# Optimization experiments

Measured on AMD Instinct MI355X. Metric: run time of the kernel, lower is better.

The kernel has to match this reference:

```python
import jax, jax.numpy as jnp
import numpy as np

D_MODEL = 768
H = 12
D_K = D_MODEL // H
D_FF = 3072
B, S = 1, 4096


def setup_inputs() -> dict:
    key = jax.random.key(0)
    ks = jax.random.split(key, 16)
    sd = 0.02
    inp = {
        'x': jax.random.normal(ks[0], (B, S, D_MODEL), jnp.float32),
        'mask': jnp.ones((B, 1, S, S), jnp.int32),
        'wq': jax.random.normal(ks[1], (D_MODEL, D_MODEL), jnp.float32) * sd,
        'bq': jnp.zeros((D_MODEL,), jnp.float32),
        'wk': jax.random.normal(ks[2], (D_MODEL, D_MODEL), jnp.float32) * sd,
        'bk': jnp.zeros((D_MODEL,), jnp.float32),
        'wv': jax.random.normal(ks[3], (D_MODEL, D_MODEL), jnp.float32) * sd,
        'bv': jnp.zeros((D_MODEL,), jnp.float32),
        'wo': jax.random.normal(ks[4], (D_MODEL, D_MODEL), jnp.float32) * sd,
        'bo': jnp.zeros((D_MODEL,), jnp.float32),
        'w1': jax.random.normal(ks[5], (D_MODEL, D_FF), jnp.float32) * sd,
        'b1': jnp.zeros((D_FF,), jnp.float32),
        'w2': jax.random.normal(ks[6], (D_FF, D_MODEL), jnp.float32) * sd,
        'b2': jnp.zeros((D_MODEL,), jnp.float32),
    }
    return inp


def _mha(x, mask, wq, bq, wk, bk, wv, bv, wo, bo):
    b, s, _ = x.shape
    q = (x @ wq + bq).reshape(b, s, H, D_K).transpose(0, 2, 1, 3)  # (b,h,s,dk)
    k = (x @ wk + bk).reshape(b, s, H, D_K).transpose(0, 2, 1, 3)
    v = (x @ wv + bv).reshape(b, s, H, D_K).transpose(0, 2, 1, 3)
    scores = jnp.einsum('bhqd,bhkd->bhqk', q, k) / jnp.sqrt(jnp.float32(D_K))
    scores = jnp.where(mask == 0, jnp.float32(-1e9), scores)
    p = jax.nn.softmax(scores, axis=-1)  # dropout disabled (eval)
    ctx = jnp.einsum('bhqk,bhkd->bhqd', p, v)
    ctx = ctx.transpose(0, 2, 1, 3).reshape(b, s, D_MODEL)
    return ctx @ wo + bo


def reference(x, mask, wq, bq, wk, bk, wv, bv, wo, bo, w1, b1, w2, b2):
    # residual 1: self-attention (SkipConnection applies no LayerNorm in forward)
    x = x + _mha(x, mask, wq, bq, wk, bk, wv, bv, wo, bo)
    # residual 2: feed-forward (relu), dropout disabled
    ff = jax.nn.relu(x @ w1 + b1) @ w2 + b2
    return x + ff
```

## Files before the change

kernel.cpp:

```cpp
#include <hip/hip_runtime.h>


typedef __attribute__((ext_vector_type(4))) float f32x4;
typedef __attribute__((ext_vector_type(8))) short bf16x8;

#define MFMA(a, b, c) __builtin_amdgcn_mfma_f32_16x16x32_bf16((a), (b), (c), 0, 0, 0)

__device__ inline ushort f2b(float f) {
  union { float f; unsigned u; } v; v.f = f;
  unsigned r = v.u + 0x7fffu + ((v.u >> 16) & 1u);
  return (ushort)(r >> 16);
}

__device__ inline unsigned cvt_pk_bf16(float lo, float hi) {
  unsigned r;
  asm("v_cvt_pk_bf16_f32 %0, %1, %2" : "=v"(r) : "v"(lo), "v"(hi));
  return r;
}

__device__ inline float fexp2(float x) {
  float r;
  asm("v_exp_f32 %0, %1" : "=v"(r) : "v"(x));
  return r;
}

__device__ inline void gl_lds16(const ushort* g, ushort* l) {
  __builtin_amdgcn_global_load_lds(
      (const __attribute__((address_space(1))) unsigned int*)g,
      (__attribute__((address_space(3))) unsigned int*)l, 16, 0, 0);
}


__global__ void cvt_f2b_kernel(const float* __restrict__ in, ushort* __restrict__ out, int n) {
  int i = (blockIdx.x * blockDim.x + threadIdx.x) * 4;
  if (i < n) {
    float4 v = *(const float4*)&in[i];
    ushort4 o; o.x = f2b(v.x); o.y = f2b(v.y); o.z = f2b(v.z); o.w = f2b(v.w);
    *(ushort4*)&out[i] = o;
  }
}

__global__ void tr_f2b_kernel(const float* __restrict__ in, ushort* __restrict__ out, int K, int N) {
  __shared__ float tile[32][33];
  const int kb = blockIdx.x * 32, nb = blockIdx.y * 32;
  const int tx = threadIdx.x, ty = threadIdx.y;
#pragma unroll
  for (int i = 0; i < 32; i += 8)
    tile[ty + i][tx] = in[(size_t)(kb + ty + i) * N + nb + tx];
  __syncthreads();
#pragma unroll
  for (int i = 0; i < 32; i += 8)
    out[(size_t)(nb + ty + i) * K + kb + tx] = f2b(tile[tx][ty + i]);
}

__global__ void concat3_kernel(const float* __restrict__ a, const float* __restrict__ b,
                               const float* __restrict__ c, float* __restrict__ o) {
  int i = blockIdx.x * 256 + threadIdx.x;
  if (i < 2304) o[i] = (i < 768) ? a[i] : (i < 1536) ? b[i - 768] : c[i - 1536];
}

template <int EPI, int BM, int BN>
__global__ __launch_bounds__(256, 2) void gemm_bt(
    const ushort* __restrict__ A, const ushort* __restrict__ Bt,
    const float* __restrict__ bias, const float* __restrict__ res,
    float* __restrict__ outF, ushort* __restrict__ outB, ushort* __restrict__ outV,
    int M, int N, int K) {
  constexpr int IM = BM / 32;
  constexpr int JN = BN / 32;
  __shared__ __align__(16) ushort As[2][BM * 32];
  __shared__ __align__(16) ushort Bs[2][BN * 32];
  const int t = threadIdx.x;
  const int wave = t >> 6, lane = t & 63;
  const int lr = lane & 15, lg = lane >> 4;
  const int wm = (wave >> 1) * (BM / 2), wn = (wave & 1) * (BN / 2);
  const int bm = blockIdx.x * BM, bn = blockIdx.y * BN;

  f32x4 acc[IM][JN] = {};

  const ushort* Ab = A + (size_t)bm * K;
  const ushort* Bb = Bt + (size_t)bn * K;
  const int srow = t >> 2;
  const int scol = (t & 3) * 8;

  auto STAGE = [&](int buf, int k0) {
#pragma unroll
    for (int rr = 0; rr < BM; rr += 64)
      gl_lds16(Ab + (size_t)(srow + rr) * K + k0 + scol, &As[buf][rr * 32 + t * 8]);
#pragma unroll
    for (int rr = 0; rr < BN; rr += 64)
      gl_lds16(Bb + (size_t)(srow + rr) * K + k0 + scol, &Bs[buf][rr * 32 + t * 8]);
  };

  STAGE(0, 0);
  __syncthreads();
  int cur = 0;

  for (int k0 = 0; k0 < K; k0 += 32) {
    if (k0 + 32 < K) STAGE(cur ^ 1, k0 + 32);

    bf16x8 af[IM], bfr[JN];
#pragma unroll
    for (int i = 0; i < IM; ++i)
      af[i] = *(const bf16x8*)&As[cur][(wm + i * 16 + lr) * 32 + lg * 8];
#pragma unroll
    for (int j = 0; j < JN; ++j)
      bfr[j] = *(const bf16x8*)&Bs[cur][(wn + j * 16 + lr) * 32 + lg * 8];
#pragma unroll
    for (int i = 0; i < IM; ++i)
#pragma unroll
      for (int j = 0; j < JN; ++j)
        acc[i][j] = MFMA(af[i], bfr[j], acc[i][j]);

    __syncthreads();
    cur ^= 1;
  }

#pragma unroll
  for (int j = 0; j < JN; ++j) {
    const int col = bn + wn + j * 16 + lr;
    const float bv = bias[col];
#pragma unroll
    for (int i = 0; i < IM; ++i) {
      const int row0 = bm + wm + i * 16 + lg * 4;
      float v[4];
#pragma unroll
      for (int r = 0; r < 4; ++r) {
        v[r] = acc[i][j][r] + bv;
        if (EPI == 2) v[r] = fmaxf(v[r], 0.f);
        if (EPI == 1 || EPI == 3) v[r] += res[(size_t)(row0 + r) * N + col];
        if (EPI == 1 || EPI == 3) outF[(size_t)(row0 + r) * N + col] = v[r];
      }
      if (EPI == 0) {
        if (col < 1536) {
#pragma unroll
          for (int r = 0; r < 4; ++r) outB[(size_t)(row0 + r) * 1536 + col] = f2b(v[r]);
        } else {
          ushort4 pk;
          pk.x = f2b(v[0]); pk.y = f2b(v[1]); pk.z = f2b(v[2]); pk.w = f2b(v[3]);
          *(ushort4*)&outV[(size_t)(col - 1536) * 4096 + row0] = pk;
        }
      } else if (EPI == 1 || EPI == 2) {
#pragma unroll
        for (int r = 0; r < 4; ++r) outB[(size_t)(row0 + r) * N + col] = f2b(v[r]);
      }
    }
  }
}

__global__ __launch_bounds__(512, 6) void attn_kernel(
    const ushort* __restrict__ qk, const ushort* __restrict__ vg,
    ushort* __restrict__ Opart, float2* __restrict__ stats) {
  __shared__ __align__(16) ushort Ks[2][64 * 64];
  __shared__ __align__(16) ushort Vt[64 * 64];
  __shared__ __align__(16) ushort Ps[8][16 * 72];
  const int h = blockIdx.y;
  const int qb = blockIdx.x * 128;
  const int kb0 = blockIdx.z * 2048;
  const int t = threadIdx.x, wave = t >> 6, lane = t & 63;
  const int lr = lane & 15, lg = lane >> 4;
  constexpr float SC = 0.18033688011112042f;

  const ushort* Qp = qk + (size_t)(qb + wave * 16 + lr) * 1536 + 64 * h;
  const bf16x8 qf0 = *(const bf16x8*)(Qp + lg * 8);
  const bf16x8 qf1 = *(const bf16x8*)(Qp + 32 + lg * 8);

  f32x4 oacc[4] = {};
  float m = -1e30f, lsum = 0.f;

  const int srow = t >> 3;
  const int schunk = ((t & 7) ^ (srow & 7)) * 8;
  const ushort* Kp0 = qk + (size_t)srow * 1536 + 768 + 64 * h + schunk;
  const ushort* Vp0 = vg + (size_t)(64 * h + srow) * 4096 + schunk;
  const int swr = lr & 7;

  auto STAGE_K = [&](int buf, int kb) {
    gl_lds16(Kp0 + (size_t)kb * 1536, &Ks[buf][t * 8]);
  };
  auto STAGE_V = [&](int kb) {
    gl_lds16(Vp0 + kb, &Vt[t * 8]);
  };

  STAGE_K(0, kb0);
  __syncthreads();
  int cur = 0;

  for (int kb = kb0; kb < kb0 + 2048; kb += 64) {
    if (kb + 64 < kb0 + 2048) STAGE_K(cur ^ 1, kb + 64);
    STAGE_V(kb);

    const ushort* Kc = Ks[cur];

    float p[16];
    __builtin_amdgcn_s_setprio(1);
#pragma unroll
    for (int kt = 0; kt < 4; ++kt) {
      const int kr = kt * 16 + lr;
      bf16x8 ka0 = *(const bf16x8*)&Kc[kr * 64 + ((lg ^ swr) * 8)];
      bf16x8 ka1 = *(const bf16x8*)&Kc[kr * 64 + (((lg + 4) ^ swr) * 8)];
      f32x4 s = {};
      s = MFMA(ka0, qf0, s);
      s = MFMA(ka1, qf1, s);
#pragma unroll
      for (int r = 0; r < 4; ++r) p[kt * 4 + r] = s[r];
    }
    __builtin_amdgcn_s_setprio(0);

    float mx = fmaxf(fmaxf(p[0], p[1]), p[2]);
    mx = fmaxf(fmaxf(mx, p[3]), p[4]);
    mx = fmaxf(fmaxf(mx, p[5]), p[6]);
    mx = fmaxf(fmaxf(mx, p[7]), p[8]);
    mx = fmaxf(fmaxf(mx, p[9]), p[10]);
    mx = fmaxf(fmaxf(mx, p[11]), p[12]);
    mx = fmaxf(fmaxf(mx, p[13]), p[14]);
    mx = fmaxf(mx, p[15]);
    mx = fmaxf(mx, __shfl_xor(mx, 16));
    mx = fmaxf(mx, __shfl_xor(mx, 32));
    mx *= SC;

    if (!__all(mx <= m + 8.0f)) {
      const float alpha = fexp2(m - mx);
      lsum *= alpha;
      float al[4];
#pragma unroll
      for (int r = 0; r < 4; ++r) al[r] = __shfl(alpha, lg * 4 + r);
#pragma unroll
      for (int dt = 0; dt < 4; ++dt)
#pragma unroll
        for (int r = 0; r < 4; ++r) oacc[dt][r] *= al[r];
      m = mx;
    }

#pragma unroll
    for (int i = 0; i < 16; ++i) p[i] = fexp2(fmaf(p[i], SC, -m));

    ushort* Pw = Ps[wave];
#pragma unroll
    for (int kt = 0; kt < 4; ++kt) {
      uint2 pk;
      pk.x = cvt_pk_bf16(p[kt * 4 + 0], p[kt * 4 + 1]);
      pk.y = cvt_pk_bf16(p[kt * 4 + 2], p[kt * 4 + 3]);
      *(uint2*)&Pw[lr * 72 + kt * 16 + lg * 4] = pk;
    }

    float ts = ((p[0] + p[1]) + (p[2] + p[3])) + ((p[4] + p[5]) + (p[6] + p[7]));
    ts += ((p[8] + p[9]) + (p[10] + p[11])) + ((p[12] + p[13]) + (p[14] + p[15]));
    ts += __shfl_xor(ts, 16);
    ts += __shfl_xor(ts, 32);
    lsum += ts;

    __syncthreads();

    bf16x8 pa0 = *(const bf16x8*)&Pw[lr * 72 + lg * 8];
    bf16x8 pa1 = *(const bf16x8*)&Pw[lr * 72 + 32 + lg * 8];
    __builtin_amdgcn_s_setprio(1);
#pragma unroll
    for (int dt = 0; dt < 4; ++dt) {
      const int vd = dt * 16 + lr;
      bf16x8 vb0 = *(const bf16x8*)&Vt[vd * 64 + ((lg ^ swr) * 8)];
      bf16x8 vb1 = *(const bf16x8*)&Vt[vd * 64 + (((lg + 4) ^ swr) * 8)];
      oacc[dt] = MFMA(pa0, vb0, oacc[dt]);
      oacc[dt] = MFMA(pa1, vb1, oacc[dt]);
    }
    __builtin_amdgcn_s_setprio(0);

    __syncthreads();
    cur ^= 1;
  }

  float li[4];
#pragma unroll
  for (int r = 0; r < 4; ++r) li[r] = __shfl(lsum, lg * 4 + r);
  ushort* Os = Opart + (size_t)blockIdx.z * 3145728;
#pragma unroll
  for (int dt = 0; dt < 4; ++dt)
#pragma unroll
    for (int r = 0; r < 4; ++r) {
      const int row = qb + wave * 16 + lg * 4 + r;
      const int col = 64 * h + dt * 16 + lr;
      Os[(size_t)row * 768 + col] = f2b(oacc[dt][r] / li[r]);
    }
  if (lane < 16) {
    float2 st; st.x = m; st.y = lsum;
    stats[(size_t)blockIdx.z * 49152 + (size_t)(qb + wave * 16 + lane) * 12 + h] = st;
  }
}

__global__ void attn_combine_kernel(const ushort* __restrict__ Op,
                                    const float2* __restrict__ st,
                                    ushort* __restrict__ ctx) {
  const int i = blockIdx.x * 256 + threadIdx.x;
  const int q = i / 96, cc = i - q * 96;
  const int h = cc >> 3;
  const float2 s0 = st[(size_t)q * 12 + h];
  const float2 s1 = st[49152 + (size_t)q * 12 + h];
  const float M = fmaxf(s0.x, s1.x);
  const float w0 = fexp2(s0.x - M) * s0.y;
  const float w1 = fexp2(s1.x - M) * s1.y;
  const float ri = 1.0f / (w0 + w1);
  const float a0 = w0 * ri, a1 = w1 * ri;
  const size_t off = (size_t)q * 768 + cc * 8;
  const uint4 ua = *(const uint4*)(Op + off);
  const uint4 ub = *(const uint4*)(Op + 3145728 + off);
  const uint* pa = (const uint*)&ua;
  const uint* pb = (const uint*)&ub;
  uint out[4];
#pragma unroll
  for (int j = 0; j < 4; ++j) {
    const float fa0 = __uint_as_float((pa[j] & 0xffffu) << 16);
    const float fa1 = __uint_as_float(pa[j] & 0xffff0000u);
    const float fb0 = __uint_as_float((pb[j] & 0xffffu) << 16);
    const float fb1 = __uint_as_float(pb[j] & 0xffff0000u);
    out[j] = cvt_pk_bf16(fa0 * a0 + fb0 * a1, fa1 * a0 + fb1 * a1);
  }
  *(uint4*)(ctx + off) = *(uint4*)&out[0];
}


extern "C" void kernel_launch(void* const* d_in, const int* in_sizes, int n_in,
                              void* d_out, int out_size, void* d_ws, size_t ws_size,
                              hipStream_t stream) {
  (void)in_sizes; (void)n_in; (void)out_size; (void)ws_size;
  const float* x  = (const float*)d_in[0];
  const float* wq = (const float*)d_in[2];
  const float* bq = (const float*)d_in[3];
  const float* wk = (const float*)d_in[4];
  const float* bk = (const float*)d_in[5];
  const float* wv = (const float*)d_in[6];
  const float* bv = (const float*)d_in[7];
  const float* wo = (const float*)d_in[8];
  const float* bo = (const float*)d_in[9];
  const float* w1 = (const float*)d_in[10];
  const float* b1 = (const float*)d_in[11];
  const float* w2 = (const float*)d_in[12];
  const float* b2 = (const float*)d_in[13];
  float* out = (float*)d_out;

  char* ws = (char*)d_ws;
  ushort* xb   = (ushort*)(ws);
  ushort* qkvt = (ushort*)(ws + 6291456);
  ushort* wot  = (ushort*)(ws + 9830400);
  ushort* w1t  = (ushort*)(ws + 11010048);
  ushort* w2t  = (ushort*)(ws + 15728640);
  float*  bqkv = (float*)(ws + 20447232);
  ushort* qkb  = (ushort*)(ws + 20456448);
  ushort* vgb  = (ushort*)(ws + 33039360);
  ushort* ctxb = (ushort*)(ws + 39330816);
  float*  x1   = (float*)(ws + 45622272);
  ushort* x1b  = (ushort*)(ws + 58205184);
  ushort* hbuf = (ushort*)(ws + 20456448);
  ushort* opart = (ushort*)(ws + 45622272);
  float2* astat = (float2*)(ws + 58205184);

  const dim3 tb(32, 8);
  cvt_f2b_kernel<<<3072, 256, 0, stream>>>(x, xb, 4096 * 768);
  tr_f2b_kernel<<<dim3(24, 24), tb, 0, stream>>>(wq, qkvt, 768, 768);
  tr_f2b_kernel<<<dim3(24, 24), tb, 0, stream>>>(wk, qkvt + 768 * 768, 768, 768);
  tr_f2b_kernel<<<dim3(24, 24), tb, 0, stream>>>(wv, qkvt + 2 * 768 * 768, 768, 768);
  tr_f2b_kernel<<<dim3(24, 24), tb, 0, stream>>>(wo, wot, 768, 768);
  tr_f2b_kernel<<<dim3(24, 96), tb, 0, stream>>>(w1, w1t, 768, 3072);
  tr_f2b_kernel<<<dim3(96, 24), tb, 0, stream>>>(w2, w2t, 3072, 768);
  concat3_kernel<<<9, 256, 0, stream>>>(bq, bk, bv, bqkv);

  gemm_bt<0, 64, 128><<<dim3(64, 18), 256, 0, stream>>>(xb, qkvt, bqkv, nullptr, nullptr, qkb, vgb, 4096, 2304, 768);
  attn_kernel<<<dim3(32, 12, 2), 512, 0, stream>>>(qkb, vgb, opart, astat);
  attn_combine_kernel<<<1536, 256, 0, stream>>>(opart, astat, ctxb);
  gemm_bt<1, 64, 64><<<dim3(64, 12), 256, 0, stream>>>(ctxb, wot, bo, x, x1, x1b, nullptr, 4096, 768, 768);
  gemm_bt<2, 128, 128><<<dim3(32, 24), 256, 0, stream>>>(x1b, w1t, b1, nullptr, nullptr, hbuf, nullptr, 4096, 3072, 768);
  gemm_bt<3, 64, 64><<<dim3(64, 12), 256, 0, stream>>>(hbuf, w2t, b2, x1, out, nullptr, nullptr, 4096, 768, 3072);
}
```

Baseline: 222.0 us.

## Double-buffer V tile in attention, drop mid-loop barrier, merge weight transposes

The attention loop now double-buffers the V tile alongside K, prefetching both for the next block. This lets the mid-iteration __syncthreads be replaced by a wave-local LDS waitcnt plus a sched barrier, since each wave only reads back its own P tile. The four 768x768 weight transpose launches are merged into one launch indexed by blockIdx.z to cut launch overhead. The cost is extra LDS per block, which may lower occupancy for the 512-thread attention kernel, and the change relies on per-wave P buffers for correctness.

```diff
diff --git a/kernel.cpp b/kernel.cpp
--- a/kernel.cpp
+++ b/kernel.cpp
@@ -51,6 +51,27 @@
 #pragma unroll
   for (int i = 0; i < 32; i += 8)
     out[(size_t)(nb + ty + i) * K + kb + tx] = f2b(tile[tx][ty + i]);
+}
+
+__global__ void tr4_f2b_kernel(const float* __restrict__ s0, const float* __restrict__ s1,
+                               const float* __restrict__ s2, const float* __restrict__ s3,
+                               ushort* __restrict__ d0, ushort* __restrict__ d1,
+                               ushort* __restrict__ d2, ushort* __restrict__ d3) {
+  __shared__ float tile[32][33];
+  const float* in; ushort* out;
+  if (blockIdx.z == 0)      { in = s0; out = d0; }
+  else if (blockIdx.z == 1) { in = s1; out = d1; }
+  else if (blockIdx.z == 2) { in = s2; out = d2; }
+  else                      { in = s3; out = d3; }
+  const int kb = blockIdx.x * 32, nb = blockIdx.y * 32;
+  const int tx = threadIdx.x, ty = threadIdx.y;
+#pragma unroll
+  for (int i = 0; i < 32; i += 8)
+    tile[ty + i][tx] = in[(size_t)(kb + ty + i) * 768 + nb + tx];
+  __syncthreads();
+#pragma unroll
+  for (int i = 0; i < 32; i += 8)
+    out[(size_t)(nb + ty + i) * 768 + kb + tx] = f2b(tile[tx][ty + i]);
 }
 
 __global__ void concat3_kernel(const float* __restrict__ a, const float* __restrict__ b,
@@ -151,7 +172,7 @@
     const ushort* __restrict__ qk, const ushort* __restrict__ vg,
     ushort* __restrict__ Opart, float2* __restrict__ stats) {
   __shared__ __align__(16) ushort Ks[2][64 * 64];
-  __shared__ __align__(16) ushort Vt[64 * 64];
+  __shared__ __align__(16) ushort Vt[2][64 * 64];
   __shared__ __align__(16) ushort Ps[8][16 * 72];
   const int h = blockIdx.y;
   const int qb = blockIdx.x * 128;
@@ -173,22 +194,20 @@
   const ushort* Vp0 = vg + (size_t)(64 * h + srow) * 4096 + schunk;
   const int swr = lr & 7;
 
-  auto STAGE_K = [&](int buf, int kb) {
+  auto STAGE = [&](int buf, int kb) {
     gl_lds16(Kp0 + (size_t)kb * 1536, &Ks[buf][t * 8]);
+    gl_lds16(Vp0 + kb, &Vt[buf][t * 8]);
   };
-  auto STAGE_V = [&](int kb) {
-    gl_lds16(Vp0 + kb, &Vt[t * 8]);
-  };
-
-  STAGE_K(0, kb0);
+
+  STAGE(0, kb0);
   __syncthreads();
   int cur = 0;
 
   for (int kb = kb0; kb < kb0 + 2048; kb += 64) {
-    if (kb + 64 < kb0 + 2048) STAGE_K(cur ^ 1, kb + 64);
-    STAGE_V(kb);
+    if (kb + 64 < kb0 + 2048) STAGE(cur ^ 1, kb + 64);
 
     const ushort* Kc = Ks[cur];
+    const ushort* Vc = Vt[cur];
 
     float p[16];
     __builtin_amdgcn_s_setprio(1);
@@ -248,7 +267,8 @@
     ts += __shfl_xor(ts, 32);
     lsum += ts;
 
-    __syncthreads();
+    asm volatile("s_waitcnt lgkmcnt(0)" ::: "memory");
+    __builtin_amdgcn_sched_barrier(0);
 
     bf16x8 pa0 = *(const bf16x8*)&Pw[lr * 72 + lg * 8];
     bf16x8 pa1 = *(const bf16x8*)&Pw[lr * 72 + 32 + lg * 8];
@@ -256,8 +276,8 @@
 #pragma unroll
     for (int dt = 0; dt < 4; ++dt) {
       const int vd = dt * 16 + lr;
-      bf16x8 vb0 = *(const bf16x8*)&Vt[vd * 64 + ((lg ^ swr) * 8)];
-      bf16x8 vb1 = *(const bf16x8*)&Vt[vd * 64 + (((lg + 4) ^ swr) * 8)];
+      bf16x8 vb0 = *(const bf16x8*)&Vc[vd * 64 + ((lg ^ swr) * 8)];
+      bf16x8 vb1 = *(const bf16x8*)&Vc[vd * 64 + (((lg + 4) ^ swr) * 8)];
       oacc[dt] = MFMA(pa0, vb0, oacc[dt]);
       oacc[dt] = MFMA(pa1, vb1, oacc[dt]);
     }
@@ -353,10 +373,8 @@
 
   const dim3 tb(32, 8);
   cvt_f2b_kernel<<<3072, 256, 0, stream>>>(x, xb, 4096 * 768);
-  tr_f2b_kernel<<<dim3(24, 24), tb, 0, stream>>>(wq, qkvt, 768, 768);
-  tr_f2b_kernel<<<dim3(24, 24), tb, 0, stream>>>(wk, qkvt + 768 * 768, 768, 768);
-  tr_f2b_kernel<<<dim3(24, 24), tb, 0, stream>>>(wv, qkvt + 2 * 768 * 768, 768, 768);
-  tr_f2b_kernel<<<dim3(24, 24), tb, 0, stream>>>(wo, wot, 768, 768);
+  tr4_f2b_kernel<<<dim3(24, 24, 4), tb, 0, stream>>>(
+      wq, wk, wv, wo, qkvt, qkvt + 768 * 768, qkvt + 2 * 768 * 768, wot);
   tr_f2b_kernel<<<dim3(24, 96), tb, 0, stream>>>(w1, w1t, 768, 3072);
   tr_f2b_kernel<<<dim3(96, 24), tb, 0, stream>>>(w2, w2t, 3072, 768);
   concat3_kernel<<<9, 256, 0, stream>>>(bq, bk, bv, bqkv);
```

Result: faster. 217.2 us (-2.2%).
